# Optimization experiments

Measured on AMD Instinct MI355X. Metric: run time of the kernel, lower is better.

The kernel has to match this reference:

```python
import jax, jax.numpy as jnp
import numpy as np

N = 100000
EMB = 64
HID = 64
E = 1600000

def _sage_conv(x, src, dst, w_l, b_l, w_r):
    # PyG SAGEConv (aggr='mean'): out_i = lin_l(mean_{j->i} x_j) + lin_r(x_i)
    msgs = x[src]                                        # [E, d] gather
    agg = jax.ops.segment_sum(msgs, dst, num_segments=N) # [N, d] scatter-add
    deg = jax.ops.segment_sum(jnp.ones((src.shape[0],), x.dtype), dst, num_segments=N)
    agg = agg / jnp.maximum(deg, 1.0)[:, None]           # mean; 0-degree nodes stay 0
    return agg @ w_l.T + b_l + x @ w_r.T                 # lin_l has bias, lin_r does not

def setup_inputs() -> dict:
    key = jax.random.key(0)
    ks = jax.random.split(key, 8)
    emb_std = 1.0 / (EMB ** 0.5)
    # Linear init (Kaiming-uniform-like bounds approximated with uniform +-1/sqrt(fan_in))
    def lin(k, out_d, in_d):
        return jax.random.uniform(k, (out_d, in_d), jnp.float32, -1.0/np.sqrt(in_d), 1.0/np.sqrt(in_d))
    return {
        "embedding": jax.random.normal(ks[0], (N, EMB), jnp.float32) * emb_std,
        "w_l0": lin(ks[1], HID, EMB),
        "b_l0": jax.random.uniform(ks[2], (HID,), jnp.float32, -1.0/np.sqrt(EMB), 1.0/np.sqrt(EMB)),
        "w_r0": lin(ks[3], HID, EMB),
        "w_l1": lin(ks[4], HID, HID),
        "b_l1": jax.random.uniform(ks[5], (HID,), jnp.float32, -1.0/np.sqrt(HID), 1.0/np.sqrt(HID)),
        "w_r1": lin(ks[6], HID, HID),
        "edge_index": jax.random.randint(ks[7], (2, E), 0, N, dtype=jnp.int64),
    }

def reference(embedding, w_l0, b_l0, w_r0, w_l1, b_l1, w_r1, edge_index):
    src, dst = edge_index[0], edge_index[1]
    x = embedding
    x = _sage_conv(x, src, dst, w_l0, b_l0, w_r0)
    x = jax.nn.relu(x)
    x = _sage_conv(x, src, dst, w_l1, b_l1, w_r1)
    # F.normalize(p=2, dim=1): x / clamp_min(||x||_2, 1e-12)
    norm = jnp.sqrt(jnp.sum(x * x, axis=1, keepdims=True))
    return x / jnp.maximum(norm, 1e-12)
```

## Files before the change

### kernel.cpp

```cpp
#include <hip/hip_runtime.h>
#include <math.h>

#define D 64
#define BSHIFT 8
#define BN 256
#define MAXB 512
#define NBLK 256
#define NBLK_LOG 8
#define SCHUNK 4096

typedef short bf16x8v __attribute__((ext_vector_type(8)));
typedef float f32x4v __attribute__((ext_vector_type(4)));

__device__ __forceinline__ unsigned short f2bf(float f) {
    unsigned u = __float_as_uint(f);
    return (unsigned short)((u + 0x7FFFu + ((u >> 16) & 1u)) >> 16);
}
__device__ __forceinline__ float bf2f(unsigned short b) {
    return __uint_as_float(((unsigned)b) << 16);
}

__global__ __launch_bounds__(256) void prep(
        const int* __restrict__ ei, int* __restrict__ flag,
        const float* __restrict__ w0, const float* __restrict__ w1,
        const float* __restrict__ w2, const float* __restrict__ w3,
        unsigned short* __restrict__ hi, unsigned short* __restrict__ lo,
        const float* __restrict__ x, uint4* __restrict__ xb4, int total8,
        int nXbfBlocks) {
    const int b = blockIdx.x;
    if (b == 0) {
        if (threadIdx.x < 64) {
            int v = ei[2 * threadIdx.x + 1];
            unsigned long long m = __ballot(v != 0);
            if (threadIdx.x == 0) flag[0] = (m == 0ULL) ? 1 : 0;
        }
        return;
    }
    if (b < 65) {
        int i = (b - 1) * 256 + threadIdx.x;
        const float* ws_[4] = {w0, w1, w2, w3};
        float f = ws_[i >> 12][i & 4095];
        unsigned short h = f2bf(f);
        hi[i] = h;
        lo[i] = f2bf(f - bf2f(h));
        return;
    }
    int i = (b - 65) * 256 + threadIdx.x;
    int stride = nXbfBlocks * 256;
    for (; i < total8; i += stride) {
        float4 u0 = *(const float4*)(x + (size_t)i * 8);
        float4 u1 = *(const float4*)(x + (size_t)i * 8 + 4);
        uint4 p;
        p.x = (unsigned)f2bf(u0.x) | ((unsigned)f2bf(u0.y) << 16);
        p.y = (unsigned)f2bf(u0.z) | ((unsigned)f2bf(u0.w) << 16);
        p.z = (unsigned)f2bf(u1.x) | ((unsigned)f2bf(u1.y) << 16);
        p.w = (unsigned)f2bf(u1.z) | ((unsigned)f2bf(u1.w) << 16);
        xb4[i] = p;
    }
}


__global__ __launch_bounds__(256) void hist2d(
        const void* __restrict__ eidx, const int* __restrict__ flagp,
        int* __restrict__ H, int nE, int nb, int epb) {
    __shared__ int h[MAXB];
    const bool idx64 = (*flagp != 0);
    const int* __restrict__ ei32 = (const int*)eidx;
    const long long* __restrict__ ei64 = (const long long*)eidx;
    for (int i = threadIdx.x; i < nb; i += 256) h[i] = 0;
    __syncthreads();
    const int e0 = blockIdx.x * epb;
    const int e1 = min(e0 + epb, nE);
    for (int e = e0 + threadIdx.x; e < e1; e += 256) {
        int d = idx64 ? (int)ei64[e + nE] : ei32[e + nE];
        atomicAdd(&h[d >> BSHIFT], 1);
    }
    __syncthreads();
    for (int i = threadIdx.x; i < nb; i += 256)
        H[(i << NBLK_LOG) + blockIdx.x] = h[i];
}

__global__ __launch_bounds__(256) void scan_h_partial(
        const int* __restrict__ H, int* __restrict__ part, int total) {
    __shared__ int red[4];
    int base = blockIdx.x * SCHUNK + threadIdx.x * 16;
    int s = 0;
    #pragma unroll
    for (int k = 0; k < 16; ++k) { int i = base + k; if (i < total) s += H[i]; }
    #pragma unroll
    for (int off = 32; off >= 1; off >>= 1) s += __shfl_xor(s, off, 64);
    int lane = threadIdx.x & 63, wid = threadIdx.x >> 6;
    if (lane == 0) red[wid] = s;
    __syncthreads();
    if (threadIdx.x == 0) part[blockIdx.x] = red[0] + red[1] + red[2] + red[3];
}

__global__ void scan_h_mid(int* __restrict__ part, int* __restrict__ bbaseN,
                           int nParts, int nE) {
    int tid = threadIdx.x;
    int v = (tid < nParts) ? part[tid] : 0;
    int x = v;
    #pragma unroll
    for (int off = 1; off < 64; off <<= 1) { int y = __shfl_up(x, off, 64); if (tid >= off) x += y; }
    if (tid < nParts) part[tid] = x - v;
    if (tid == 0) bbaseN[0] = nE;
}

__global__ __launch_bounds__(256) void scan_h_final(
        int* __restrict__ H, const int* __restrict__ part,
        int* __restrict__ bbase, int total) {
    __shared__ int wtot[4];
    int tid = threadIdx.x, lane = tid & 63, wid = tid >> 6;
    int base = blockIdx.x * SCHUNK + tid * 16;
    int v[16]; int t = 0;
    #pragma unroll
    for (int k = 0; k < 16; ++k) { int i = base + k; v[k] = (i < total) ? H[i] : 0; t += v[k]; }
    int x = t;
    #pragma unroll
    for (int off = 1; off < 64; off <<= 1) { int y = __shfl_up(x, off, 64); if (lane >= off) x += y; }
    if (lane == 63) wtot[wid] = x;
    __syncthreads();
    int woff = 0;
    for (int w = 0; w < wid; ++w) woff += wtot[w];
    int run = part[blockIdx.x] + woff + (x - t);
    #pragma unroll
    for (int k = 0; k < 16; ++k) {
        int i = base + k;
        if (i < total) {
            H[i] = run;
            if ((i & (NBLK - 1)) == 0) bbase[i >> NBLK_LOG] = run;
            run += v[k];
        }
    }
}

__global__ __launch_bounds__(256) void fill2(
        const void* __restrict__ eidx, const int* __restrict__ flagp,
        const int* __restrict__ H, unsigned* __restrict__ pairs,
        int nE, int nb, int epb) {
    __shared__ int cur[MAXB];
    const bool idx64 = (*flagp != 0);
    const int* __restrict__ ei32 = (const int*)eidx;
    const long long* __restrict__ ei64 = (const long long*)eidx;
    for (int i = threadIdx.x; i < nb; i += 256)
        cur[i] = H[(i << NBLK_LOG) + blockIdx.x];
    __syncthreads();
    const int e0 = blockIdx.x * epb;
    const int e1 = min(e0 + epb, nE);
    for (int e = e0 + threadIdx.x; e < e1; e += 256) {
        int s, d;
        if (idx64) { s = (int)ei64[e]; d = (int)ei64[e + nE]; }
        else       { s = ei32[e];      d = ei32[e + nE]; }
        int pos = atomicAdd(&cur[d >> BSHIFT], 1);
        pairs[pos] = (unsigned)s | ((unsigned)(d & (BN - 1)) << 20);
    }
}

__global__ __launch_bounds__(256) void bucket_to_csr(
        const unsigned* __restrict__ pairs,
        const int* __restrict__ bbase,
        int* __restrict__ rowStart, int* __restrict__ srcs,
        int N, int nb, int nE) {
    __shared__ int lcnt[BN];
    __shared__ int lcur[BN];
    __shared__ int wtot[4];
    const int b = blockIdx.x;
    const int base = bbase[b];
    const int cnt  = bbase[b + 1] - base;
    const int tid = threadIdx.x, lane = tid & 63, wid = tid >> 6;
    lcnt[tid] = 0;
    __syncthreads();
    for (int i = tid; i < cnt; i += 256)
        atomicAdd(&lcnt[(int)(pairs[base + i] >> 20)], 1);
    __syncthreads();
    int v = lcnt[tid];
    int x = v;
    #pragma unroll
    for (int off = 1; off < 64; off <<= 1) { int y = __shfl_up(x, off, 64); if (lane >= off) x += y; }
    if (lane == 63) wtot[wid] = x;
    __syncthreads();
    if (tid == 0) {
        int r = 0;
        for (int w = 0; w < 4; ++w) { int t = wtot[w]; wtot[w] = r; r += t; }
    }
    __syncthreads();
    int excl = wtot[wid] + (x - v);
    lcur[tid] = excl;
    int node = b * BN + tid;
    if (node < N) rowStart[node] = base + excl;
    if (b == nb - 1 && tid == 0) rowStart[N] = nE;
    __syncthreads();
    for (int i = tid; i < cnt; i += 256) {
        unsigned p = pairs[base + i];
        int pos = atomicAdd(&lcur[(int)(p >> 20)], 1);
        srcs[base + pos] = (int)(p & 0xFFFFFu);
    }
}

#define UNPK8(v, arr)                                                     \
    do {                                                                  \
        arr[0] += __uint_as_float((v).x << 16);                           \
        arr[1] += __uint_as_float((v).x & 0xFFFF0000u);                   \
        arr[2] += __uint_as_float((v).y << 16);                           \
        arr[3] += __uint_as_float((v).y & 0xFFFF0000u);                   \
        arr[4] += __uint_as_float((v).z << 16);                           \
        arr[5] += __uint_as_float((v).z & 0xFFFF0000u);                   \
        arr[6] += __uint_as_float((v).w << 16);                           \
        arr[7] += __uint_as_float((v).w & 0xFFFF0000u);                   \
    } while (0)

__global__ __launch_bounds__(256) void gather_mean_bf16(
        const unsigned short* __restrict__ xb,
        const int* __restrict__ rowStart,
        const int* __restrict__ srcs,
        unsigned short* __restrict__ aggb,
        int nNodes) {
    const int tid = threadIdx.x;
    const int gl = tid & 7;
    const int grp = tid >> 3;
    const int node = blockIdx.x * 32 + grp;
    if (node >= nNodes) return;
    const int r0 = rowStart[node], r1 = rowStart[node + 1];
    float a[8] = {0.f,0.f,0.f,0.f,0.f,0.f,0.f,0.f};
    const unsigned short* xp = xb + gl * 8;
    int j = r0;
    for (; j + 8 <= r1; j += 8) {
        uint4 v0 = *(const uint4*)(xp + (size_t)srcs[j    ] * D);
        uint4 v1 = *(const uint4*)(xp + (size_t)srcs[j + 1] * D);
        uint4 v2 = *(const uint4*)(xp + (size_t)srcs[j + 2] * D);
        uint4 v3 = *(const uint4*)(xp + (size_t)srcs[j + 3] * D);
        uint4 v4 = *(const uint4*)(xp + (size_t)srcs[j + 4] * D);
        uint4 v5 = *(const uint4*)(xp + (size_t)srcs[j + 5] * D);
        uint4 v6 = *(const uint4*)(xp + (size_t)srcs[j + 6] * D);
        uint4 v7 = *(const uint4*)(xp + (size_t)srcs[j + 7] * D);
        UNPK8(v0, a); UNPK8(v1, a); UNPK8(v2, a); UNPK8(v3, a);
        UNPK8(v4, a); UNPK8(v5, a); UNPK8(v6, a); UNPK8(v7, a);
    }
    if (j + 4 <= r1) {
        uint4 v0 = *(const uint4*)(xp + (size_t)srcs[j    ] * D);
        uint4 v1 = *(const uint4*)(xp + (size_t)srcs[j + 1] * D);
        uint4 v2 = *(const uint4*)(xp + (size_t)srcs[j + 2] * D);
        uint4 v3 = *(const uint4*)(xp + (size_t)srcs[j + 3] * D);
        UNPK8(v0, a); UNPK8(v1, a); UNPK8(v2, a); UNPK8(v3, a);
        j += 4;
    }
    if (j + 2 <= r1) {
        uint4 v0 = *(const uint4*)(xp + (size_t)srcs[j    ] * D);
        uint4 v1 = *(const uint4*)(xp + (size_t)srcs[j + 1] * D);
        UNPK8(v0, a); UNPK8(v1, a);
        j += 2;
    }
    if (j < r1) {
        uint4 v = *(const uint4*)(xp + (size_t)srcs[j] * D);
        UNPK8(v, a);
    }
    const float inv = 1.0f / fmaxf((float)(r1 - r0), 1.0f);
    uint4 p;
    p.x = (unsigned)f2bf(a[0]*inv) | ((unsigned)f2bf(a[1]*inv) << 16);
    p.y = (unsigned)f2bf(a[2]*inv) | ((unsigned)f2bf(a[3]*inv) << 16);
    p.z = (unsigned)f2bf(a[4]*inv) | ((unsigned)f2bf(a[5]*inv) << 16);
    p.w = (unsigned)f2bf(a[6]*inv) | ((unsigned)f2bf(a[7]*inv) << 16);
    *(uint4*)(aggb + (size_t)node * D + gl * 8) = p;
}

template<int LAYER>
__global__ __launch_bounds__(256) void gemm_mfma(
        const unsigned short* __restrict__ aggb,
        const unsigned short* __restrict__ xin,
        const unsigned short* __restrict__ wHi,
        const unsigned short* __restrict__ wLo,
        const float* __restrict__ bl,
        float* __restrict__ outf,
        unsigned short* __restrict__ outb,
        int nNodes) {
    const int l = threadIdx.x & 63;
    const int wv = threadIdx.x >> 6;
    const int col = l & 15, grp = l >> 4;
    const int base0 = blockIdx.x * 128 + wv * 32;
    if (base0 >= nNodes) return;

    bf16x8v gH[2][2], sH[2][2];
    #pragma unroll
    for (int tt = 0; tt < 2; ++tt) {
        const int anode = min(base0 + tt * 16 + col, nNodes - 1);
        #pragma unroll
        for (int h = 0; h < 2; ++h) {
            gH[tt][h] = *(const bf16x8v*)(aggb + (size_t)anode * D + h * 32 + grp * 8);
            sH[tt][h] = *(const bf16x8v*)(xin  + (size_t)anode * D + h * 32 + grp * 8);
        }
    }

    f32x4v acc[2][4];
    #pragma unroll
    for (int tt = 0; tt < 2; ++tt)
        #pragma unroll
        for (int t = 0; t < 4; ++t) acc[tt][t] = (f32x4v){0.f, 0.f, 0.f, 0.f};

    #pragma unroll
    for (int t = 0; t < 4; ++t) {
        const unsigned short* whl = wHi + (size_t)(t * 16 + col) * D;
        const unsigned short* wol = wLo + (size_t)(t * 16 + col) * D;
        const unsigned short* whr = whl + 4096;
        const unsigned short* wor = wol + 4096;
        #pragma unroll
        for (int h = 0; h < 2; ++h) {
            const int k0 = h * 32 + grp * 8;
            bf16x8v bh  = *(const bf16x8v*)(whl + k0);
            bf16x8v bo  = *(const bf16x8v*)(wol + k0);
            bf16x8v bh2 = *(const bf16x8v*)(whr + k0);
            bf16x8v bo2 = *(const bf16x8v*)(wor + k0);
            #pragma unroll
            for (int tt = 0; tt < 2; ++tt) {
                acc[tt][t] = __builtin_amdgcn_mfma_f32_16x16x32_bf16(gH[tt][h], bh,  acc[tt][t], 0, 0, 0);
                acc[tt][t] = __builtin_amdgcn_mfma_f32_16x16x32_bf16(gH[tt][h], bo,  acc[tt][t], 0, 0, 0);
                acc[tt][t] = __builtin_amdgcn_mfma_f32_16x16x32_bf16(sH[tt][h], bh2, acc[tt][t], 0, 0, 0);
                acc[tt][t] = __builtin_amdgcn_mfma_f32_16x16x32_bf16(sH[tt][h], bo2, acc[tt][t], 0, 0, 0);
            }
        }
    }

    #pragma unroll
    for (int tt = 0; tt < 2; ++tt) {
        const int base = base0 + tt * 16;
        #pragma unroll
        for (int t = 0; t < 4; ++t) {
            float b = bl[t * 16 + col];
            #pragma unroll
            for (int r = 0; r < 4; ++r) acc[tt][t][r] += b;
        }
        if (LAYER == 0) {
            #pragma unroll
            for (int t = 0; t < 4; ++t)
                #pragma unroll
                for (int r = 0; r < 4; ++r) {
                    int n = base + grp * 4 + r;
                    if (n < nNodes)
                        outb[(size_t)n * D + t * 16 + col] = f2bf(fmaxf(acc[tt][t][r], 0.f));
                }
        } else {
            float ss[4] = {0.f, 0.f, 0.f, 0.f};
            #pragma unroll
            for (int t = 0; t < 4; ++t)
                #pragma unroll
                for (int r = 0; r < 4; ++r) ss[r] += acc[tt][t][r] * acc[tt][t][r];
            #pragma unroll
            for (int r = 0; r < 4; ++r) {
                #pragma unroll
                for (int off = 1; off < 16; off <<= 1) ss[r] += __shfl_xor(ss[r], off, 64);
            }
            float inv[4];
            #pragma unroll
            for (int r = 0; r < 4; ++r) inv[r] = 1.0f / fmaxf(sqrtf(ss[r]), 1e-12f);
            #pragma unroll
            for (int t = 0; t < 4; ++t)
                #pragma unroll
                for (int r = 0; r < 4; ++r) {
                    int n = base + grp * 4 + r;
                    if (n < nNodes)
                        outf[(size_t)n * D + t * 16 + col] = acc[tt][t][r] * inv[r];
                }
        }
    }
}


__global__ void detect_idx64(const int* __restrict__ ei, int* __restrict__ flag) {
    int v = ei[2 * threadIdx.x + 1];
    unsigned long long b = __ballot(v != 0);
    if (threadIdx.x == 0) flag[0] = (b == 0ULL) ? 1 : 0;
}

__global__ __launch_bounds__(256) void sage_scatter(
        const float* __restrict__ x,
        const void* __restrict__ eidx,
        const int* __restrict__ flagp,
        float* __restrict__ agg,
        float* __restrict__ deg,
        int nE, int doDeg) {
    const bool idx64 = (*flagp != 0);
    const int lane = threadIdx.x & 63;
    int wave = (int)((blockIdx.x * blockDim.x + threadIdx.x) >> 6);
    const int waveStride = (int)((gridDim.x * blockDim.x) >> 6);
    const int* __restrict__ ei32 = (const int*)eidx;
    const long long* __restrict__ ei64 = (const long long*)eidx;
    for (int e = wave; e < nE; e += waveStride) {
        int s, d;
        if (idx64) { s = (int)ei64[e]; d = (int)ei64[e + nE]; }
        else       { s = ei32[e];      d = ei32[e + nE]; }
        atomicAdd(&agg[(size_t)d * D + lane], x[(size_t)s * D + lane]);
        if (doDeg && lane == 0) atomicAdd(&deg[d], 1.0f);
    }
}

__global__ __launch_bounds__(256) void sage_update(
        const float* __restrict__ xin,
        const float* __restrict__ agg,
        const float* __restrict__ deg,
        const float* __restrict__ wl,
        const float* __restrict__ bl,
        const float* __restrict__ wr,
        float* __restrict__ xout,
        int nNodes, int mode) {
    __shared__ float wlT[D * D];
    __shared__ float wrT[D * D];
    __shared__ float rowA[4][D];
    __shared__ float rowX[4][D];
    for (int i = threadIdx.x; i < D * D; i += blockDim.x) {
        int f = i >> 6, k = i & 63;
        wlT[k * D + f] = wl[i];
        wrT[k * D + f] = wr[i];
    }
    __syncthreads();
    const int lane = threadIdx.x & 63;
    const int wid = threadIdx.x >> 6;
    const float blv = bl[lane];
    for (int node = blockIdx.x * 4 + wid; node < nNodes; node += gridDim.x * 4) {
        float dg = fmaxf(deg[node], 1.0f);
        float a  = agg[(size_t)node * D + lane] / dg;
        float xv = xin[(size_t)node * D + lane];
        rowA[wid][lane] = a;
        rowX[wid][lane] = xv;
        float acc = blv;
        #pragma unroll
        for (int k = 0; k < D; ++k) {
            acc = fmaf(rowA[wid][k], wlT[k * D + lane], acc);
            acc = fmaf(rowX[wid][k], wrT[k * D + lane], acc);
        }
        if (mode == 0) {
            xout[(size_t)node * D + lane] = fmaxf(acc, 0.0f);
        } else {
            float ss = acc * acc;
            #pragma unroll
            for (int off = 32; off >= 1; off >>= 1) ss += __shfl_xor(ss, off, 64);
            xout[(size_t)node * D + lane] = acc / fmaxf(sqrtf(ss), 1e-12f);
        }
    }
}

extern "C" void kernel_launch(void* const* d_in, const int* in_sizes, int n_in,
                              void* d_out, int out_size, void* d_ws, size_t ws_size,
                              hipStream_t stream) {
    const float* x   = (const float*)d_in[0];
    const float* wl0 = (const float*)d_in[1];
    const float* bl0 = (const float*)d_in[2];
    const float* wr0 = (const float*)d_in[3];
    const float* wl1 = (const float*)d_in[4];
    const float* bl1 = (const float*)d_in[5];
    const float* wr1 = (const float*)d_in[6];
    const void*  ei  = d_in[7];
    float* out = (float*)d_out;

    const int N = in_sizes[0] / D;
    const int E = in_sizes[7] / 2;
    const int NB = (N + BN - 1) / BN;
    const int EPB = (E + NBLK - 1) / NBLK;
    const int TOTAL = NB << NBLK_LOG;
    const int NPARTS = (TOTAL + SCHUNK - 1) / SCHUNK;

    char* ws = (char*)d_ws;
    size_t off = 0;
    auto alloc = [&](size_t bytes) { void* p = ws + off; off = (off + bytes + 255) & ~(size_t)255; return p; };

    size_t need = 0;
    {
        size_t o = 0;
        auto sim = [&](size_t b) { o = (o + b + 255) & ~(size_t)255; };
        sim(4); sim(16384 * 2); sim(16384 * 2);
        sim(((size_t)MAXB << NBLK_LOG) * 4); sim(64 * 4); sim(((size_t)MAXB + 1) * 4);
        sim(((size_t)N + 1) * 4); sim((size_t)E * 4); sim((size_t)E * 4);
        sim((size_t)N * D * 2); sim((size_t)N * D * 2); sim((size_t)N * D * 2);
        need = o;
    }

    if (ws_size >= need && NB <= MAXB && NPARTS <= 64) {
        int* flag     = (int*)alloc(4);
        unsigned short* whi = (unsigned short*)alloc(16384 * 2);
        unsigned short* wlo = (unsigned short*)alloc(16384 * 2);
        int* H        = (int*)alloc(((size_t)MAXB << NBLK_LOG) * 4);
        int* part     = (int*)alloc(64 * 4);
        int* bbase    = (int*)alloc(((size_t)MAXB + 1) * 4);
        int* rowStart = (int*)alloc(((size_t)N + 1) * 4);
        int* srcs     = (int*)alloc((size_t)E * 4);
        unsigned* pairs = (unsigned*)alloc((size_t)E * 4);
        unsigned short* xb   = (unsigned short*)alloc((size_t)N * D * 2);
        unsigned short* x1b  = (unsigned short*)alloc((size_t)N * D * 2);
        unsigned short* aggb = (unsigned short*)alloc((size_t)N * D * 2);

        const int nXbf = 1024;
        prep<<<65 + nXbf, 256, 0, stream>>>((const int*)ei, flag,
                                            wl0, wr0, wl1, wr1, whi, wlo,
                                            x, (uint4*)xb, N * 8, nXbf);
        hist2d<<<NBLK, 256, 0, stream>>>(ei, flag, H, E, NB, EPB);
        scan_h_partial<<<NPARTS, 256, 0, stream>>>(H, part, TOTAL);
        scan_h_mid<<<1, 64, 0, stream>>>(part, &bbase[NB], NPARTS, E);
        scan_h_final<<<NPARTS, 256, 0, stream>>>(H, part, bbase, TOTAL);
        fill2<<<NBLK, 256, 0, stream>>>(ei, flag, H, pairs, E, NB, EPB);
        bucket_to_csr<<<NB, 256, 0, stream>>>(pairs, bbase, rowStart, srcs, N, NB, E);

        const int gGather = (N + 31) / 32;
        const int gMfma   = (N + 127) / 128;
        gather_mean_bf16<<<gGather, 256, 0, stream>>>(xb, rowStart, srcs, aggb, N);
        gemm_mfma<0><<<gMfma, 256, 0, stream>>>(aggb, xb, whi, wlo, bl0,
                                                (float*)0, x1b, N);
        gather_mean_bf16<<<gGather, 256, 0, stream>>>(x1b, rowStart, srcs, aggb, N);
        gemm_mfma<1><<<gMfma, 256, 0, stream>>>(aggb, x1b, whi + 2 * 4096, wlo + 2 * 4096,
                                                bl1, out, (unsigned short*)0, N);
    } else {
        int*   flag = (int*)alloc(4);
        float* deg  = (float*)alloc((size_t)N * 4);
        float* agg  = (float*)alloc((size_t)N * D * 4);
        float* x1   = out;

        detect_idx64<<<1, 64, 0, stream>>>((const int*)ei, flag);
        hipMemsetAsync(deg, 0, ((size_t)N + (size_t)N * D) * 4, stream);
        sage_scatter<<<4096, 256, 0, stream>>>(x, ei, flag, agg, deg, E, 1);
        sage_update<<<2048, 256, 0, stream>>>(x, agg, deg, wl0, bl0, wr0, x1, N, 0);
        hipMemsetAsync(agg, 0, (size_t)N * D * 4, stream);
        sage_scatter<<<4096, 256, 0, stream>>>(x1, ei, flag, agg, deg, E, 0);
        sage_update<<<2048, 256, 0, stream>>>(x1, agg, deg, wl1, bl1, wr1, out, N, 1);
    }
}
```

Baseline: 169.8 us.

## Merge prep with histogram, fold mid-scan into final scan, widen GEMM tiles

The index-width flag is now computed inline with a wave ballot in each kernel that needs it, so the weight/feature conversion and the destination histogram can share one launch. The separate one-block mid-scan kernel is removed: each final-scan block recomputes the prefix over the partial sums itself. The MFMA GEMM now gives each wave 64 nodes instead of 32, halving the grid and reusing each weight fragment load across more tiles. Together these cut two kernel launches and their dependency gaps, at the cost of more registers in the GEMM and redundant flag and prefix work per block.

```diff
diff --git a/kernel.cpp b/kernel.cpp
--- a/kernel.cpp
+++ b/kernel.cpp
@@ -8,6 +8,7 @@
 #define NBLK 256
 #define NBLK_LOG 8
 #define SCHUNK 4096
+#define NXBF 1024
 
 typedef short bf16x8v __attribute__((ext_vector_type(8)));
 typedef float f32x4v __attribute__((ext_vector_type(4)));
@@ -20,24 +21,21 @@
     return __uint_as_float(((unsigned)b) << 16);
 }
 
-__global__ __launch_bounds__(256) void prep(
-        const int* __restrict__ ei, int* __restrict__ flag,
+__device__ __forceinline__ bool is_idx64(const int* __restrict__ ei32) {
+    int v = ei32[2 * (threadIdx.x & 63) + 1];
+    return __ballot(v != 0) == 0ULL;
+}
+
+__global__ __launch_bounds__(256) void prep_hist(
         const float* __restrict__ w0, const float* __restrict__ w1,
         const float* __restrict__ w2, const float* __restrict__ w3,
         unsigned short* __restrict__ hi, unsigned short* __restrict__ lo,
         const float* __restrict__ x, uint4* __restrict__ xb4, int total8,
-        int nXbfBlocks) {
+        const void* __restrict__ eidx, int* __restrict__ H,
+        int nE, int nb, int epb) {
     const int b = blockIdx.x;
-    if (b == 0) {
-        if (threadIdx.x < 64) {
-            int v = ei[2 * threadIdx.x + 1];
-            unsigned long long m = __ballot(v != 0);
-            if (threadIdx.x == 0) flag[0] = (m == 0ULL) ? 1 : 0;
-        }
-        return;
-    }
-    if (b < 65) {
-        int i = (b - 1) * 256 + threadIdx.x;
+    if (b < 64) {
+        int i = b * 256 + threadIdx.x;
         const float* ws_[4] = {w0, w1, w2, w3};
         float f = ws_[i >> 12][i & 4095];
         unsigned short h = f2bf(f);
@@ -45,31 +43,29 @@
         lo[i] = f2bf(f - bf2f(h));
         return;
     }
-    int i = (b - 65) * 256 + threadIdx.x;
-    int stride = nXbfBlocks * 256;
-    for (; i < total8; i += stride) {
-        float4 u0 = *(const float4*)(x + (size_t)i * 8);
-        float4 u1 = *(const float4*)(x + (size_t)i * 8 + 4);
-        uint4 p;
-        p.x = (unsigned)f2bf(u0.x) | ((unsigned)f2bf(u0.y) << 16);
-        p.y = (unsigned)f2bf(u0.z) | ((unsigned)f2bf(u0.w) << 16);
-        p.z = (unsigned)f2bf(u1.x) | ((unsigned)f2bf(u1.y) << 16);
-        p.w = (unsigned)f2bf(u1.z) | ((unsigned)f2bf(u1.w) << 16);
-        xb4[i] = p;
-    }
-}
-
-
-__global__ __launch_bounds__(256) void hist2d(
-        const void* __restrict__ eidx, const int* __restrict__ flagp,
-        int* __restrict__ H, int nE, int nb, int epb) {
+    if (b < 64 + NXBF) {
+        int i = (b - 64) * 256 + threadIdx.x;
+        int stride = NXBF * 256;
+        for (; i < total8; i += stride) {
+            float4 u0 = *(const float4*)(x + (size_t)i * 8);
+            float4 u1 = *(const float4*)(x + (size_t)i * 8 + 4);
+            uint4 p;
+            p.x = (unsigned)f2bf(u0.x) | ((unsigned)f2bf(u0.y) << 16);
+            p.y = (unsigned)f2bf(u0.z) | ((unsigned)f2bf(u0.w) << 16);
+            p.z = (unsigned)f2bf(u1.x) | ((unsigned)f2bf(u1.y) << 16);
+            p.w = (unsigned)f2bf(u1.z) | ((unsigned)f2bf(u1.w) << 16);
+            xb4[i] = p;
+        }
+        return;
+    }
     __shared__ int h[MAXB];
-    const bool idx64 = (*flagp != 0);
+    const int hb = b - (64 + NXBF);
     const int* __restrict__ ei32 = (const int*)eidx;
     const long long* __restrict__ ei64 = (const long long*)eidx;
+    const bool idx64 = is_idx64(ei32);
     for (int i = threadIdx.x; i < nb; i += 256) h[i] = 0;
     __syncthreads();
-    const int e0 = blockIdx.x * epb;
+    const int e0 = hb * epb;
     const int e1 = min(e0 + epb, nE);
     for (int e = e0 + threadIdx.x; e < e1; e += 256) {
         int d = idx64 ? (int)ei64[e + nE] : ei32[e + nE];
@@ -77,8 +73,9 @@
     }
     __syncthreads();
     for (int i = threadIdx.x; i < nb; i += 256)
-        H[(i << NBLK_LOG) + blockIdx.x] = h[i];
-}
+        H[(i << NBLK_LOG) + hb] = h[i];
+}
+
 
 __global__ __launch_bounds__(256) void scan_h_partial(
         const int* __restrict__ H, int* __restrict__ part, int total) {
@@ -95,22 +92,17 @@
     if (threadIdx.x == 0) part[blockIdx.x] = red[0] + red[1] + red[2] + red[3];
 }
 
-__global__ void scan_h_mid(int* __restrict__ part, int* __restrict__ bbaseN,
-                           int nParts, int nE) {
-    int tid = threadIdx.x;
-    int v = (tid < nParts) ? part[tid] : 0;
-    int x = v;
-    #pragma unroll
-    for (int off = 1; off < 64; off <<= 1) { int y = __shfl_up(x, off, 64); if (tid >= off) x += y; }
-    if (tid < nParts) part[tid] = x - v;
-    if (tid == 0) bbaseN[0] = nE;
-}
-
 __global__ __launch_bounds__(256) void scan_h_final(
         int* __restrict__ H, const int* __restrict__ part,
-        int* __restrict__ bbase, int total) {
+        int* __restrict__ bbase, int total, int nParts, int nb, int nE) {
     __shared__ int wtot[4];
     int tid = threadIdx.x, lane = tid & 63, wid = tid >> 6;
+    int pv = (lane < nParts) ? part[lane] : 0;
+    int px = pv;
+    #pragma unroll
+    for (int off = 1; off < 64; off <<= 1) { int y = __shfl_up(px, off, 64); if (lane >= off) px += y; }
+    int blockOff = (blockIdx.x == 0) ? 0 : __shfl(px, blockIdx.x - 1, 64);
+
     int base = blockIdx.x * SCHUNK + tid * 16;
     int v[16]; int t = 0;
     #pragma unroll
@@ -122,7 +114,7 @@
     __syncthreads();
     int woff = 0;
     for (int w = 0; w < wid; ++w) woff += wtot[w];
-    int run = part[blockIdx.x] + woff + (x - t);
+    int run = blockOff + woff + (x - t);
     #pragma unroll
     for (int k = 0; k < 16; ++k) {
         int i = base + k;
@@ -132,16 +124,17 @@
             run += v[k];
         }
     }
+    if (blockIdx.x == 0 && tid == 0) bbase[nb] = nE;
 }
 
 __global__ __launch_bounds__(256) void fill2(
-        const void* __restrict__ eidx, const int* __restrict__ flagp,
+        const void* __restrict__ eidx,
         const int* __restrict__ H, unsigned* __restrict__ pairs,
         int nE, int nb, int epb) {
     __shared__ int cur[MAXB];
-    const bool idx64 = (*flagp != 0);
     const int* __restrict__ ei32 = (const int*)eidx;
     const long long* __restrict__ ei64 = (const long long*)eidx;
+    const bool idx64 = is_idx64(ei32);
     for (int i = threadIdx.x; i < nb; i += 256)
         cur[i] = H[(i << NBLK_LOG) + blockIdx.x];
     __syncthreads();
@@ -276,12 +269,12 @@
     const int l = threadIdx.x & 63;
     const int wv = threadIdx.x >> 6;
     const int col = l & 15, grp = l >> 4;
-    const int base0 = blockIdx.x * 128 + wv * 32;
+    const int base0 = blockIdx.x * 256 + wv * 64;
     if (base0 >= nNodes) return;
 
-    bf16x8v gH[2][2], sH[2][2];
-    #pragma unroll
-    for (int tt = 0; tt < 2; ++tt) {
+    bf16x8v gH[4][2], sH[4][2];
+    #pragma unroll
+    for (int tt = 0; tt < 4; ++tt) {
         const int anode = min(base0 + tt * 16 + col, nNodes - 1);
         #pragma unroll
         for (int h = 0; h < 2; ++h) {
@@ -290,9 +283,9 @@
         }
     }
 
-    f32x4v acc[2][4];
-    #pragma unroll
-    for (int tt = 0; tt < 2; ++tt)
+    f32x4v acc[4][4];
+    #pragma unroll
+    for (int tt = 0; tt < 4; ++tt)
         #pragma unroll
         for (int t = 0; t < 4; ++t) acc[tt][t] = (f32x4v){0.f, 0.f, 0.f, 0.f};
 
@@ -310,7 +303,7 @@
             bf16x8v bh2 = *(const bf16x8v*)(whr + k0);
             bf16x8v bo2 = *(const bf16x8v*)(wor + k0);
             #pragma unroll
-            for (int tt = 0; tt < 2; ++tt) {
+            for (int tt = 0; tt < 4; ++tt) {
                 acc[tt][t] = __builtin_amdgcn_mfma_f32_16x16x32_bf16(gH[tt][h], bh,  acc[tt][t], 0, 0, 0);
                 acc[tt][t] = __builtin_amdgcn_mfma_f32_16x16x32_bf16(gH[tt][h], bo,  acc[tt][t], 0, 0, 0);
                 acc[tt][t] = __builtin_amdgcn_mfma_f32_16x16x32_bf16(sH[tt][h], bh2, acc[tt][t], 0, 0, 0);
@@ -320,7 +313,7 @@
     }
 
     #pragma unroll
-    for (int tt = 0; tt < 2; ++tt) {
+    for (int tt = 0; tt < 4; ++tt) {
         const int base = base0 + tt * 16;
         #pragma unroll
         for (int t = 0; t < 4; ++t) {
@@ -485,20 +478,19 @@
         unsigned short* xb   = (unsigned short*)alloc((size_t)N * D * 2);
         unsigned short* x1b  = (unsigned short*)alloc((size_t)N * D * 2);
         unsigned short* aggb = (unsigned short*)alloc((size_t)N * D * 2);
-
-        const int nXbf = 1024;
-        prep<<<65 + nXbf, 256, 0, stream>>>((const int*)ei, flag,
-                                            wl0, wr0, wl1, wr1, whi, wlo,
-                                            x, (uint4*)xb, N * 8, nXbf);
-        hist2d<<<NBLK, 256, 0, stream>>>(ei, flag, H, E, NB, EPB);
+        (void)flag;
+
+        prep_hist<<<64 + NXBF + NBLK, 256, 0, stream>>>(
+            wl0, wr0, wl1, wr1, whi, wlo,
+            x, (uint4*)xb, N * 8,
+            ei, H, E, NB, EPB);
         scan_h_partial<<<NPARTS, 256, 0, stream>>>(H, part, TOTAL);
-        scan_h_mid<<<1, 64, 0, stream>>>(part, &bbase[NB], NPARTS, E);
-        scan_h_final<<<NPARTS, 256, 0, stream>>>(H, part, bbase, TOTAL);
-        fill2<<<NBLK, 256, 0, stream>>>(ei, flag, H, pairs, E, NB, EPB);
+        scan_h_final<<<NPARTS, 256, 0, stream>>>(H, part, bbase, TOTAL, NPARTS, NB, E);
+        fill2<<<NBLK, 256, 0, stream>>>(ei, H, pairs, E, NB, EPB);
         bucket_to_csr<<<NB, 256, 0, stream>>>(pairs, bbase, rowStart, srcs, N, NB, E);
 
         const int gGather = (N + 31) / 32;
-        const int gMfma   = (N + 127) / 128;
+        const int gMfma   = (N + 255) / 256;
         gather_mean_bf16<<<gGather, 256, 0, stream>>>(xb, rowStart, srcs, aggb, N);
         gemm_mfma<0><<<gMfma, 256, 0, stream>>>(aggb, xb, whi, wlo, bl0,
                                                 (float*)0, x1b, N);
```

Result: faster. 153.5 us (-9.6%).
